# Kernel tuning notes

Hardware: AMD Instinct MI355X
Metric: run time of the kernel (lower is better)

## Reference

```python
import jax, jax.numpy as jnp
import numpy as np

N_NODES = 100000
N_EDGES = 1600000
IN_C, HID_C, OUT_C = 128, 256, 256


def sage_conv(x, src, dst, W_l, b_l, W_r, n_nodes):
    # mean aggregation of source-node features onto destination nodes
    msg_sum = jax.ops.segment_sum(x[src], dst, num_segments=n_nodes)  # [N, F]
    deg = jax.ops.segment_sum(jnp.ones_like(dst, dtype=x.dtype), dst, num_segments=n_nodes)
    aggr = msg_sum / jnp.maximum(deg, 1.0)[:, None]
    # PyG SAGEConv: lin_l(aggr) (with bias) + lin_r(x) (no bias)
    return aggr @ W_l + b_l + x @ W_r


def setup_inputs() -> dict:
    key = jax.random.key(0)
    ks = jax.random.split(key, 12)
    x = jax.random.normal(ks[0], (N_NODES, IN_C), dtype=jnp.float32)
    edge_src = jax.random.randint(ks[1], (N_EDGES,), 0, N_NODES)
    edge_dst = jax.random.randint(ks[2], (N_EDGES,), 0, N_NODES)

    def glorot(k, fan_in, fan_out):
        s = jnp.sqrt(2.0 / (fan_in + fan_out)).astype(jnp.float32)
        return jax.random.normal(k, (fan_in, fan_out), dtype=jnp.float32) * s

    return {
        "x": x,
        "W_l0": glorot(ks[3], IN_C, HID_C), "b_l0": jnp.zeros((HID_C,), jnp.float32),
        "W_r0": glorot(ks[4], IN_C, HID_C),
        "W_l1": glorot(ks[5], HID_C, HID_C), "b_l1": jnp.zeros((HID_C,), jnp.float32),
        "W_r1": glorot(ks[6], HID_C, HID_C),
        "W_l2": glorot(ks[7], HID_C, OUT_C), "b_l2": jnp.zeros((OUT_C,), jnp.float32),
        "W_r2": glorot(ks[8], HID_C, OUT_C),
        "edge_src": edge_src,
        "edge_dst": edge_dst,
    }


def reference(x, W_l0, b_l0, W_r0, W_l1, b_l1, W_r1, W_l2, b_l2, W_r2, edge_src, edge_dst):
    n = x.shape[0]
    h = sage_conv(x, edge_src, edge_dst, W_l0, b_l0, W_r0, n)
    h = jax.nn.relu(h)  # dropout p=0.0 -> identity
    h = sage_conv(h, edge_src, edge_dst, W_l1, b_l1, W_r1, n)
    h = jax.nn.relu(h)
    h = sage_conv(h, edge_src, edge_dst, W_l2, b_l2, W_r2, n)
    return h
```

## Files before the change

kernel.cpp:

```cpp
#include <hip/hip_runtime.h>
#include <cstdint>
#include <cstddef>


#define N_NODES 100000
#define N_EDGES 1600000

#define SCAN_BLOCKS 256
#define SCAN_T 256

typedef unsigned short ushort;
typedef unsigned int uint;
typedef __attribute__((ext_vector_type(8))) short short8;
typedef __attribute__((ext_vector_type(4))) float floatx4;

#define AS1 __attribute__((address_space(1)))
#define AS3 __attribute__((address_space(3)))

__device__ __forceinline__ float bf2f(ushort h) {
    union { uint u; float f; } c; c.u = ((uint)h) << 16; return c.f;
}
__device__ __forceinline__ ushort f2bf(float f) {
    union { float f; uint u; } c; c.f = f;
    uint u = c.u;
    return (ushort)((u + 0x7FFFu + ((u >> 16) & 1u)) >> 16);
}


__global__ void count_edges(const int* __restrict__ dst, int* __restrict__ cnt) {
    int i = blockIdx.x * blockDim.x + threadIdx.x;
    if (i < N_EDGES) atomicAdd(&cnt[dst[i]], 1);
}

__global__ __launch_bounds__(SCAN_T) void scan_partial(
    const int* __restrict__ cnt, int* __restrict__ bsum, int n)
{
    int chunk = (n + SCAN_BLOCKS - 1) / SCAN_BLOCKS;
    int beg = blockIdx.x * chunk;
    int end = beg + chunk; if (end > n) end = n;
    int t = threadIdx.x;
    int s = 0;
    for (int i = beg + t; i < end; i += SCAN_T) s += cnt[i];
    __shared__ int sh[SCAN_T];
    sh[t] = s;
    __syncthreads();
    for (int off = SCAN_T / 2; off > 0; off >>= 1) {
        if (t < off) sh[t] += sh[t + off];
        __syncthreads();
    }
    if (t == 0) bsum[blockIdx.x] = sh[0];
}

__global__ __launch_bounds__(SCAN_T) void scan_block_sums(int* __restrict__ bsum) {
    int t = threadIdx.x;
    __shared__ int sh[SCAN_T];
    int v = bsum[t];
    sh[t] = v;
    __syncthreads();
    for (int off = 1; off < SCAN_T; off <<= 1) {
        int u = (t >= off) ? sh[t - off] : 0;
        __syncthreads();
        sh[t] += u;
        __syncthreads();
    }
    bsum[t] = sh[t] - v;
}

__global__ __launch_bounds__(SCAN_T) void scan_fill(
    int* __restrict__ cnt, const int* __restrict__ bsum,
    int* __restrict__ row_ptr, int n)
{
    int chunk = (n + SCAN_BLOCKS - 1) / SCAN_BLOCKS;
    int beg = blockIdx.x * chunk;
    int end = beg + chunk; if (end > n) end = n;
    int t = threadIdx.x;
    int per = (chunk + SCAN_T - 1) / SCAN_T;
    int tb = beg + t * per;
    int te = tb + per; if (te > end) te = end;
    int s = 0;
    for (int i = tb; i < te; ++i) s += cnt[i];
    __shared__ int sh[SCAN_T];
    sh[t] = s;
    __syncthreads();
    for (int off = 1; off < SCAN_T; off <<= 1) {
        int u = (t >= off) ? sh[t - off] : 0;
        __syncthreads();
        sh[t] += u;
        __syncthreads();
    }
    int running = bsum[blockIdx.x] + sh[t] - s;
    for (int i = tb; i < te; ++i) {
        int c = cnt[i];
        row_ptr[i] = running;
        cnt[i] = running;
        running += c;
    }
    if (blockIdx.x == 0 && t == 0) row_ptr[n] = N_EDGES;
}

__global__ void fill_csr(const int* __restrict__ src, const int* __restrict__ dst,
                         int* __restrict__ cursor, int* __restrict__ col_idx) {
    int i = blockIdx.x * blockDim.x + threadIdx.x;
    if (i < N_EDGES) {
        int p = atomicAdd(&cursor[dst[i]], 1);
        col_idx[p] = src[i];
    }
}


__global__ void convert_x_bf16(const float* __restrict__ x, ushort* __restrict__ xb, int n4) {
    int i = blockIdx.x * blockDim.x + threadIdx.x;
    if (i >= n4) return;
    float4 v = *(const float4*)&x[(size_t)i * 4];
    ushort4 o;
    o.x = f2bf(v.x); o.y = f2bf(v.y); o.z = f2bf(v.z); o.w = f2bf(v.w);
    *(ushort4*)&xb[(size_t)i * 4] = o;
}

__global__ void transpose_w_bf16(const float* __restrict__ W, ushort* __restrict__ Wt, int kshift) {
    int i = blockIdx.x * blockDim.x + threadIdx.x;
    int K = 1 << kshift;
    if (i >= 256 * K) return;
    int n = i >> kshift;
    int k = i & (K - 1);
    Wt[i] = f2bf(W[k * 256 + n]);
}

__global__ __launch_bounds__(64) void aggregate_bf16(
    const ushort* __restrict__ xb, const int* __restrict__ row_ptr,
    const int* __restrict__ col_idx, ushort* __restrict__ outb, int F)
{
    int node = blockIdx.x;
    int t = threadIdx.x;
    int b = row_ptr[node], e = row_ptr[node + 1];
    float d = (float)(e - b); if (d < 1.f) d = 1.f;
    float inv = 1.f / d;

    if (F == 256) {
        int c = t * 4;
        float a0 = 0.f, a1 = 0.f, a2 = 0.f, a3 = 0.f;
        float b0 = 0.f, b1 = 0.f, b2 = 0.f, b3 = 0.f;
        int i = b;
        for (; i + 1 < e; i += 2) {
            int s0 = col_idx[i];
            int s1 = col_idx[i + 1];
            uint2 v0 = *(const uint2*)&xb[(size_t)s0 * 256 + c];
            uint2 v1 = *(const uint2*)&xb[(size_t)s1 * 256 + c];
            a0 += bf2f((ushort)(v0.x & 0xffff)); a1 += bf2f((ushort)(v0.x >> 16));
            a2 += bf2f((ushort)(v0.y & 0xffff)); a3 += bf2f((ushort)(v0.y >> 16));
            b0 += bf2f((ushort)(v1.x & 0xffff)); b1 += bf2f((ushort)(v1.x >> 16));
            b2 += bf2f((ushort)(v1.y & 0xffff)); b3 += bf2f((ushort)(v1.y >> 16));
        }
        if (i < e) {
            int s0 = col_idx[i];
            uint2 v0 = *(const uint2*)&xb[(size_t)s0 * 256 + c];
            a0 += bf2f((ushort)(v0.x & 0xffff)); a1 += bf2f((ushort)(v0.x >> 16));
            a2 += bf2f((ushort)(v0.y & 0xffff)); a3 += bf2f((ushort)(v0.y >> 16));
        }
        ushort4 o;
        o.x = f2bf((a0 + b0) * inv); o.y = f2bf((a1 + b1) * inv);
        o.z = f2bf((a2 + b2) * inv); o.w = f2bf((a3 + b3) * inv);
        *(ushort4*)&outb[(size_t)node * 256 + c] = o;
    } else {
        int c = t * 2;
        float a0 = 0.f, a1 = 0.f, b0 = 0.f, b1 = 0.f;
        int i = b;
        for (; i + 1 < e; i += 2) {
            int s0 = col_idx[i];
            int s1 = col_idx[i + 1];
            uint v0 = *(const uint*)&xb[(size_t)s0 * 128 + c];
            uint v1 = *(const uint*)&xb[(size_t)s1 * 128 + c];
            a0 += bf2f((ushort)(v0 & 0xffff)); a1 += bf2f((ushort)(v0 >> 16));
            b0 += bf2f((ushort)(v1 & 0xffff)); b1 += bf2f((ushort)(v1 >> 16));
        }
        if (i < e) {
            int s0 = col_idx[i];
            uint v0 = *(const uint*)&xb[(size_t)s0 * 128 + c];
            a0 += bf2f((ushort)(v0 & 0xffff)); a1 += bf2f((ushort)(v0 >> 16));
        }
        ushort2 o;
        o.x = f2bf((a0 + b0) * inv); o.y = f2bf((a1 + b1) * inv);
        *(ushort2*)&outb[(size_t)node * 128 + c] = o;
    }
}

__global__ __launch_bounds__(256) void gemm_dual_mfma(
    const ushort* __restrict__ A1, const ushort* __restrict__ W1t,
    const ushort* __restrict__ A2, const ushort* __restrict__ W2t,
    const float* __restrict__ bias, ushort* __restrict__ out_bf,
    float* __restrict__ out_f32, int M, int K, int relu)
{
    __shared__ __align__(16) ushort As[4 * 64 * 8];
    __shared__ __align__(16) ushort Bs[4 * 256 * 8];
    int tid = threadIdx.x;
    int w = tid >> 6;
    int lane = tid & 63;
    int row0 = blockIdx.x * 64;

    floatx4 acc[16];
#pragma unroll
    for (int t = 0; t < 16; ++t) acc[t] = (floatx4){0.f, 0.f, 0.f, 0.f};

    int arow = row0 + lane;
    if (arow >= M) arow = M - 1;
    int ncol = w * 64 + lane;

    int m_ = lane & 15;
    int ko = lane >> 4;

    for (int mm = 0; mm < 2; ++mm) {
        const ushort* __restrict__ A = mm ? A2 : A1;
        const ushort* __restrict__ W = mm ? W2t : W1t;
        for (int k0 = 0; k0 < K; k0 += 32) {
            __builtin_amdgcn_global_load_lds(
                (const AS1 uint*)&A[(size_t)arow * K + k0 + w * 8],
                (AS3 uint*)&As[w * 512], 16, 0, 0);
#pragma unroll
            for (int j = 0; j < 4; ++j) {
                __builtin_amdgcn_global_load_lds(
                    (const AS1 uint*)&W[(size_t)ncol * K + k0 + j * 8],
                    (AS3 uint*)&Bs[(j * 256 + w * 64) * 8], 16, 0, 0);
            }
            __syncthreads();
            short8 af = *(const short8*)&As[(ko * 64 + w * 16 + m_) * 8];
#pragma unroll
            for (int t = 0; t < 16; ++t) {
                short8 bf = *(const short8*)&Bs[(ko * 256 + t * 16 + m_) * 8];
                acc[t] = __builtin_amdgcn_mfma_f32_16x16x32_bf16(af, bf, acc[t], 0, 0, 0);
            }
            __syncthreads();
        }
    }

    int mq = lane >> 4;
#pragma unroll
    for (int t = 0; t < 16; ++t) {
        int col = t * 16 + m_;
        float bv = bias[col];
#pragma unroll
        for (int r = 0; r < 4; ++r) {
            int row = row0 + w * 16 + mq * 4 + r;
            if (row >= M) continue;
            float v = acc[t][r] + bv;
            if (relu) v = fmaxf(v, 0.f);
            if (out_f32) out_f32[(size_t)row * 256 + col] = v;
            else         out_bf[(size_t)row * 256 + col] = f2bf(v);
        }
    }
}


extern "C" void kernel_launch(void* const* d_in, const int* in_sizes, int n_in,
                              void* d_out, int out_size, void* d_ws, size_t ws_size,
                              hipStream_t stream) {
    const float* x    = (const float*)d_in[0];
    const float* W_l0 = (const float*)d_in[1];
    const float* b_l0 = (const float*)d_in[2];
    const float* W_r0 = (const float*)d_in[3];
    const float* W_l1 = (const float*)d_in[4];
    const float* b_l1 = (const float*)d_in[5];
    const float* W_r1 = (const float*)d_in[6];
    const float* W_l2 = (const float*)d_in[7];
    const float* b_l2 = (const float*)d_in[8];
    const float* W_r2 = (const float*)d_in[9];
    const int* esrc   = (const int*)d_in[10];
    const int* edst   = (const int*)d_in[11];
    float* out = (float*)d_out;

    size_t off = 0;
    char* ws = (char*)d_ws;
    auto take = [&](size_t bytes) -> void* {
        void* p = ws + off;
        off += (bytes + 255) & ~(size_t)255;
        return p;
    };
    int*    cnt     = (int*)take((size_t)N_NODES * 4);
    int*    row_ptr = (int*)take((size_t)(N_NODES + 1) * 4);
    int*    col_idx = (int*)take((size_t)N_EDGES * 4);
    int*    bsum    = (int*)take((size_t)SCAN_BLOCKS * 4);
    ushort* xb      = (ushort*)take((size_t)N_NODES * 128 * 2);
    ushort* Wl0t    = (ushort*)take((size_t)256 * 128 * 2);
    ushort* Wr0t    = (ushort*)take((size_t)256 * 128 * 2);
    ushort* Wl1t    = (ushort*)take((size_t)256 * 256 * 2);
    ushort* Wr1t    = (ushort*)take((size_t)256 * 256 * 2);
    ushort* Wl2t    = (ushort*)take((size_t)256 * 256 * 2);
    ushort* Wr2t    = (ushort*)take((size_t)256 * 256 * 2);
    ushort* aggrb   = (ushort*)take((size_t)N_NODES * 256 * 2);
    ushort* ha      = (ushort*)take((size_t)N_NODES * 256 * 2);
    ushort* hb      = (ushort*)take((size_t)N_NODES * 256 * 2);
    (void)ws_size; (void)in_sizes; (void)n_in; (void)out_size;

    hipMemsetAsync(cnt, 0, (size_t)N_NODES * 4, stream);
    int eb = (N_EDGES + 255) / 256;
    count_edges<<<eb, 256, 0, stream>>>(edst, cnt);
    scan_partial<<<SCAN_BLOCKS, SCAN_T, 0, stream>>>(cnt, bsum, N_NODES);
    scan_block_sums<<<1, SCAN_T, 0, stream>>>(bsum);
    scan_fill<<<SCAN_BLOCKS, SCAN_T, 0, stream>>>(cnt, bsum, row_ptr, N_NODES);
    fill_csr<<<eb, 256, 0, stream>>>(esrc, edst, cnt, col_idx);

    int n4 = (N_NODES * 128) / 4;
    convert_x_bf16<<<(n4 + 255) / 256, 256, 0, stream>>>(x, xb, n4);
    transpose_w_bf16<<<(256 * 128 + 255) / 256, 256, 0, stream>>>(W_l0, Wl0t, 7);
    transpose_w_bf16<<<(256 * 128 + 255) / 256, 256, 0, stream>>>(W_r0, Wr0t, 7);
    transpose_w_bf16<<<(256 * 256 + 255) / 256, 256, 0, stream>>>(W_l1, Wl1t, 8);
    transpose_w_bf16<<<(256 * 256 + 255) / 256, 256, 0, stream>>>(W_r1, Wr1t, 8);
    transpose_w_bf16<<<(256 * 256 + 255) / 256, 256, 0, stream>>>(W_l2, Wl2t, 8);
    transpose_w_bf16<<<(256 * 256 + 255) / 256, 256, 0, stream>>>(W_r2, Wr2t, 8);

    dim3 ggrid((N_NODES + 63) / 64, 1);

    aggregate_bf16<<<N_NODES, 64, 0, stream>>>(xb, row_ptr, col_idx, aggrb, 128);
    gemm_dual_mfma<<<ggrid, 256, 0, stream>>>(aggrb, Wl0t, xb, Wr0t, b_l0,
                                              ha, nullptr, N_NODES, 128, 1);
    aggregate_bf16<<<N_NODES, 64, 0, stream>>>(ha, row_ptr, col_idx, aggrb, 256);
    gemm_dual_mfma<<<ggrid, 256, 0, stream>>>(aggrb, Wl1t, ha, Wr1t, b_l1,
                                              hb, nullptr, N_NODES, 256, 1);
    aggregate_bf16<<<N_NODES, 64, 0, stream>>>(hb, row_ptr, col_idx, aggrb, 256);
    gemm_dual_mfma<<<ggrid, 256, 0, stream>>>(aggrb, Wl2t, hb, Wr2t, b_l2,
                                              nullptr, out, N_NODES, 256, 0);
}
```

Baseline: 962.4 us.

## Keep weight slice resident in LDS for GEMM and partition CSR fill by destination range

```diff
diff --git a/kernel.cpp b/kernel.cpp
--- a/kernel.cpp
+++ b/kernel.cpp
@@ -8,6 +8,7 @@
 
 #define SCAN_BLOCKS 256
 #define SCAN_T 256
+#define FILL_PASSES 4
 
 typedef unsigned short ushort;
 typedef unsigned int uint;
@@ -101,8 +102,12 @@
 __global__ void fill_csr(const int* __restrict__ src, const int* __restrict__ dst,
                          int* __restrict__ cursor, int* __restrict__ col_idx) {
     int i = blockIdx.x * blockDim.x + threadIdx.x;
-    if (i < N_EDGES) {
-        int p = atomicAdd(&cursor[dst[i]], 1);
+    if (i >= N_EDGES) return;
+    int lo = (int)blockIdx.y * (N_NODES / FILL_PASSES);
+    int hi = lo + (N_NODES / FILL_PASSES);
+    int d = dst[i];
+    if (d >= lo && d < hi) {
+        int p = atomicAdd(&cursor[d], 1);
         col_idx[p] = src[i];
     }
 }
@@ -184,67 +189,81 @@
     }
 }
 
-__global__ __launch_bounds__(256) void gemm_dual_mfma(
+__global__ __launch_bounds__(512, 4) void gemm_wres(
     const ushort* __restrict__ A1, const ushort* __restrict__ W1t,
     const ushort* __restrict__ A2, const ushort* __restrict__ W2t,
     const float* __restrict__ bias, ushort* __restrict__ out_bf,
     float* __restrict__ out_f32, int M, int K, int relu)
 {
-    __shared__ __align__(16) ushort As[4 * 64 * 8];
-    __shared__ __align__(16) ushort Bs[4 * 256 * 8];
+    __shared__ __align__(16) ushort Wl[32 * 128 * 8];
     int tid = threadIdx.x;
-    int w = tid >> 6;
-    int lane = tid & 63;
-    int row0 = blockIdx.x * 64;
-
-    floatx4 acc[16];
-#pragma unroll
-    for (int t = 0; t < 16; ++t) acc[t] = (floatx4){0.f, 0.f, 0.f, 0.f};
-
-    int arow = row0 + lane;
-    if (arow >= M) arow = M - 1;
-    int ncol = w * 64 + lane;
-
-    int m_ = lane & 15;
-    int ko = lane >> 4;
+    int w = tid >> 6, lane = tid & 63;
+    int m_ = lane & 15, koq = lane >> 4;
+    int c0 = blockIdx.y * 128;
+    int row0 = blockIdx.x * 256;
+    int KQ = K >> 3;
+    int nj = (KQ * 128) >> 9;
+    int nk = K >> 5;
+
+    floatx4 acc[2][8];
+#pragma unroll
+    for (int i = 0; i < 2; ++i)
+#pragma unroll
+        for (int f = 0; f < 8; ++f) acc[i][f] = (floatx4){0.f, 0.f, 0.f, 0.f};
+
+    int ra = row0 + w * 32 + m_;      if (ra > M - 1) ra = M - 1;
+    int rb = row0 + w * 32 + 16 + m_; if (rb > M - 1) rb = M - 1;
 
     for (int mm = 0; mm < 2; ++mm) {
-        const ushort* __restrict__ A = mm ? A2 : A1;
-        const ushort* __restrict__ W = mm ? W2t : W1t;
-        for (int k0 = 0; k0 < K; k0 += 32) {
+        const ushort* __restrict__ A  = mm ? A2 : A1;
+        const ushort* __restrict__ Wt = mm ? W2t : W1t;
+        if (mm) __syncthreads();
+        for (int j = 0; j < nj; ++j) {
+            int s = j * 512 + tid;
+            int q = s >> 7, col = s & 127;
             __builtin_amdgcn_global_load_lds(
-                (const AS1 uint*)&A[(size_t)arow * K + k0 + w * 8],
-                (AS3 uint*)&As[w * 512], 16, 0, 0);
-#pragma unroll
-            for (int j = 0; j < 4; ++j) {
-                __builtin_amdgcn_global_load_lds(
-                    (const AS1 uint*)&W[(size_t)ncol * K + k0 + j * 8],
-                    (AS3 uint*)&Bs[(j * 256 + w * 64) * 8], 16, 0, 0);
+                (const AS1 uint*)&Wt[(size_t)(c0 + col) * K + q * 8],
+                (AS3 uint*)&Wl[(size_t)(j * 512 + w * 64) * 8], 16, 0, 0);
+        }
+        __syncthreads();
+
+        const ushort* __restrict__ Aa = &A[(size_t)ra * K + koq * 8];
+        const ushort* __restrict__ Ab = &A[(size_t)rb * K + koq * 8];
+
+        short8 a0 = *(const short8*)&Aa[0];
+        short8 a1 = *(const short8*)&Ab[0];
+        for (int kk = 0; kk < nk; ++kk) {
+            short8 n0, n1;
+            if (kk + 1 < nk) {
+                n0 = *(const short8*)&Aa[(kk + 1) * 32];
+                n1 = *(const short8*)&Ab[(kk + 1) * 32];
             }
-            __syncthreads();
-            short8 af = *(const short8*)&As[(ko * 64 + w * 16 + m_) * 8];
-#pragma unroll
-            for (int t = 0; t < 16; ++t) {
-                short8 bf = *(const short8*)&Bs[(ko * 256 + t * 16 + m_) * 8];
-                acc[t] = __builtin_amdgcn_mfma_f32_16x16x32_bf16(af, bf, acc[t], 0, 0, 0);
+            const ushort* bbase = &Wl[(size_t)((kk * 4 + koq) * 128 + m_) * 8];
+#pragma unroll
+            for (int fc = 0; fc < 8; ++fc) {
+                short8 b = *(const short8*)&bbase[fc * 128];
+                acc[0][fc] = __builtin_amdgcn_mfma_f32_16x16x32_bf16(a0, b, acc[0][fc], 0, 0, 0);
+                acc[1][fc] = __builtin_amdgcn_mfma_f32_16x16x32_bf16(a1, b, acc[1][fc], 0, 0, 0);
             }
-            __syncthreads();
-        }
-    }
-
-    int mq = lane >> 4;
-#pragma unroll
-    for (int t = 0; t < 16; ++t) {
-        int col = t * 16 + m_;
-        float bv = bias[col];
-#pragma unroll
-        for (int r = 0; r < 4; ++r) {
-            int row = row0 + w * 16 + mq * 4 + r;
-            if (row >= M) continue;
-            float v = acc[t][r] + bv;
-            if (relu) v = fmaxf(v, 0.f);
-            if (out_f32) out_f32[(size_t)row * 256 + col] = v;
-            else         out_bf[(size_t)row * 256 + col] = f2bf(v);
+            a0 = n0; a1 = n1;
+        }
+    }
+
+#pragma unroll
+    for (int m2 = 0; m2 < 2; ++m2) {
+#pragma unroll
+        for (int fc = 0; fc < 8; ++fc) {
+            int col = c0 + fc * 16 + m_;
+            float bv = bias[col];
+#pragma unroll
+            for (int r = 0; r < 4; ++r) {
+                int row = row0 + w * 32 + m2 * 16 + koq * 4 + r;
+                if (row >= M) continue;
+                float v = acc[m2][fc][r] + bv;
+                if (relu) v = fmaxf(v, 0.f);
+                if (out_f32) out_f32[(size_t)row * 256 + col] = v;
+                else         out_bf [(size_t)row * 256 + col] = f2bf(v);
+            }
         }
     }
 }
@@ -296,7 +315,7 @@
     scan_partial<<<SCAN_BLOCKS, SCAN_T, 0, stream>>>(cnt, bsum, N_NODES);
     scan_block_sums<<<1, SCAN_T, 0, stream>>>(bsum);
     scan_fill<<<SCAN_BLOCKS, SCAN_T, 0, stream>>>(cnt, bsum, row_ptr, N_NODES);
-    fill_csr<<<eb, 256, 0, stream>>>(esrc, edst, cnt, col_idx);
+    fill_csr<<<dim3(eb, FILL_PASSES), 256, 0, stream>>>(esrc, edst, cnt, col_idx);
 
     int n4 = (N_NODES * 128) / 4;
     convert_x_bf16<<<(n4 + 255) / 256, 256, 0, stream>>>(x, xb, n4);
@@ -307,15 +326,15 @@
     transpose_w_bf16<<<(256 * 256 + 255) / 256, 256, 0, stream>>>(W_l2, Wl2t, 8);
     transpose_w_bf16<<<(256 * 256 + 255) / 256, 256, 0, stream>>>(W_r2, Wr2t, 8);
 
-    dim3 ggrid((N_NODES + 63) / 64, 1);
+    dim3 ggrid((N_NODES + 255) / 256, 2);
 
     aggregate_bf16<<<N_NODES, 64, 0, stream>>>(xb, row_ptr, col_idx, aggrb, 128);
-    gemm_dual_mfma<<<ggrid, 256, 0, stream>>>(aggrb, Wl0t, xb, Wr0t, b_l0,
-                                              ha, nullptr, N_NODES, 128, 1);
+    gemm_wres<<<ggrid, 512, 0, stream>>>(aggrb, Wl0t, xb, Wr0t, b_l0,
+                                         ha, nullptr, N_NODES, 128, 1);
     aggregate_bf16<<<N_NODES, 64, 0, stream>>>(ha, row_ptr, col_idx, aggrb, 256);
-    gemm_dual_mfma<<<ggrid, 256, 0, stream>>>(aggrb, Wl1t, ha, Wr1t, b_l1,
-                                              hb, nullptr, N_NODES, 256, 1);
+    gemm_wres<<<ggrid, 512, 0, stream>>>(aggrb, Wl1t, ha, Wr1t, b_l1,
+                                         hb, nullptr, N_NODES, 256, 1);
     aggregate_bf16<<<N_NODES, 64, 0, stream>>>(hb, row_ptr, col_idx, aggrb, 256);
-    gemm_dual_mfma<<<ggrid, 256, 0, stream>>>(aggrb, Wl2t, hb, Wr2t, b_l2,
-                                              nullptr, out, N_NODES, 256, 0);
-}
+    gemm_wres<<<ggrid, 512, 0, stream>>>(aggrb, Wl2t, hb, Wr2t, b_l2,
+                                         nullptr, out, N_NODES, 256, 0);
+}
```

New measurement: 807.8 us. -16.1%, faster.
